# Kernel tuning notes

Hardware: AMD Instinct MI355X
Metric: run time of the kernel (lower is better)

## Reference

```python
import jax, jax.numpy as jnp
import numpy as np

M, N, E, IN, C, HID, TOPK = 4, 50000, 400000, 128, 128, 256, 2
NEG_SLOPE = 0.2


def setup_inputs() -> dict:
    key = jax.random.key(0)
    k = jax.random.split(key, 16)
    s = lambda f: 1.0 / np.sqrt(f)
    return {
        "x_src": jax.random.normal(k[0], (M, N, IN), jnp.float32),
        "x_dst": jax.random.normal(k[1], (N, IN), jnp.float32),
        "src_idx": jax.random.randint(k[2], (M, E), 0, N),
        "dst_idx": jax.random.randint(k[3], (M, E), 0, N),
        "proj_Ws": jax.random.normal(k[4], (M, IN, C), jnp.float32) * s(IN),
        "proj_bs": jnp.zeros((M, C), jnp.float32),
        "projd_W": jax.random.normal(k[5], (IN, C), jnp.float32) * s(IN),
        "projd_b": jnp.zeros((C,), jnp.float32),
        "lin_src": jax.random.normal(k[6], (M, C), jnp.float32) * s(C),
        "lin_dst": jax.random.normal(k[7], (M, C), jnp.float32) * s(C),
        "gm_W1": jax.random.normal(k[8], (C, C), jnp.float32) * s(C),
        "gm_b1": jnp.zeros((C,), jnp.float32),
        "gm_W2": jax.random.normal(k[9], (C, C), jnp.float32) * s(C),
        "gm_b2": jnp.zeros((C,), jnp.float32),
        "gate_W1": jax.random.normal(k[10], (M * C, HID), jnp.float32) * s(M * C),
        "gate_b1": jnp.zeros((HID,), jnp.float32),
        "gate_W2": jax.random.normal(k[11], (HID, M), jnp.float32) * s(HID),
        "gate_b2": jnp.zeros((M,), jnp.float32),
        "exp_W1": jax.random.normal(k[12], (M, C, HID), jnp.float32) * s(C),
        "exp_b1": jnp.zeros((M, HID), jnp.float32),
        "exp_W2": jax.random.normal(k[13], (M, HID, C), jnp.float32) * s(HID),
        "exp_b2": jnp.zeros((M, C), jnp.float32),
    }


def _propagate(xs_t, asrc_t, adst_t, si, di, recept_t):
    # GAT-style attention message passing for one edge type.
    # xs_t: [N,C] projected src feats, asrc_t/adst_t: [N] attn logits,
    # si/di: [E] edge endpoints, recept_t: [N] per-dst-node receptivity gate.
    e = jax.nn.leaky_relu(asrc_t[si] + adst_t[di], NEG_SLOPE)  # [E]
    emax = jax.ops.segment_max(e, di, num_segments=N)
    ez = jnp.exp(e - emax[di])
    den = jax.ops.segment_sum(ez, di, num_segments=N)
    alpha = ez / (den[di] + 1e-16)                             # softmax per dst node
    msg = xs_t[si] * (alpha * recept_t[di])[:, None]           # [E,C]
    return jax.ops.segment_sum(msg, di, num_segments=N)       # [N,C]


def reference(x_src, x_dst, src_idx, dst_idx, proj_Ws, proj_bs, projd_W, projd_b,
              lin_src, lin_dst, gm_W1, gm_b1, gm_W2, gm_b2,
              gate_W1, gate_b1, gate_W2, gate_b2,
              exp_W1, exp_b1, exp_W2, exp_b2):
    # --- SynapticConvLayer (eval path, heads=1) ---
    xs = jnp.einsum('mni,mic->mnc', x_src, proj_Ws) + proj_bs[:, None, :]  # [M,N,C]
    xd = x_dst @ projd_W + projd_b                                          # [N,C]
    a_src = jnp.einsum('mnc,mc->mn', xs, lin_src)
    a_dst = jnp.einsum('nc,mc->mn', xd[None].repeat(M, 0) * 0 + xd[None], lin_dst) if False else jnp.einsum('nc,mc->mn', xd, lin_dst)
    prop = jax.vmap(_propagate)
    out1 = prop(xs, a_src, a_dst, src_idx, dst_idx, jnp.ones((M, N), xs.dtype))
    # receptivity from grad_map surrogate (inference branch)
    feat_diff = out1 - xd[None]                                            # [M,N,C]
    mo = jax.nn.sigmoid(jax.nn.relu(feat_diff @ gm_W1 + gm_b1) @ gm_W2 + gm_b2)
    gd = (mo * feat_diff).mean(axis=-1)                                    # [M,N]
    recept = gd / (jnp.abs(gd) + 1e-8)                                     # L2-norm over the singleton head dim == abs
    out2 = prop(xs, a_src, a_dst, src_idx, dst_idx, recept)
    feats = jax.nn.relu(out2)                                              # [M,N,C] per-edge-type dst features
    # --- SourceExpertMoE ---
    feats_nm = feats.transpose(1, 0, 2)                                    # [N,M,C]
    gate_in = feats_nm.reshape(N, M * C)
    logits = jax.nn.relu(gate_in @ gate_W1 + gate_b1) @ gate_W2 + gate_b2
    gw = jax.nn.softmax(logits, axis=1)
    scores = gw + recept.T                                                 # gate weights + receptivity
    top_w, top_i = jax.lax.top_k(scores, TOPK)
    top_w = top_w / top_w.sum(axis=1, keepdims=True)
    # expert e applied to source-e features for every node (dense, then gather top-k)
    h = jax.nn.relu(jnp.einsum('nmi,mih->nmh', feats_nm, exp_W1) + exp_b1)
    out_all = jnp.einsum('nmh,mho->nmo', h, exp_W2) + exp_b2               # [N,M,C]
    sel = jnp.take_along_axis(out_all, top_i[:, :, None], axis=1)          # [N,K,C]
    final = (sel * top_w[:, :, None]).sum(axis=1)                          # [N,C]
    return final
```

## Files before the change

kernel.cpp:

```cpp
#include <hip/hip_runtime.h>
#include <hip/hip_bf16.h>
#include <math.h>

#define M_  4
#define N_  50000
#define E_  400000
#define IN_ 128
#define C_  128
#define HID_ 256

template<int AMODE, int EPI, int ASCALE>
__global__ void __launch_bounds__(256) gemm7(
    const float* A, const float* A2, const float* __restrict__ B,
    const float* __restrict__ bias, float* Cmat,
    const float* __restrict__ rowscale, const int* __restrict__ idx,
    const int* __restrict__ cnts, const float* __restrict__ AS,
    const float* __restrict__ fdbuf,
    int R, int K, int NC,
    long long aBatch, long long bBatch, int biasBatch, long long cBatch,
    long long strideM)
{
  __shared__ float As[8][128];
  __shared__ float Bs[8][128];
  __shared__ float red[(EPI == 5) ? 128 * 17 : 1];

  const int tid = threadIdx.x;
  const int b = blockIdx.y;
  const int Reff = cnts ? cnts[0] : R;
  const int rb = blockIdx.x * 128;
  if (rb >= Reff) return;
  const int cb = blockIdx.z * 128;

  const float* Ab = (AMODE == 2) ? A : (A + (long long)b * aBatch);
  const float* Bb = B + (long long)b * bBatch + cb;
  const float* biasb = bias + (long long)b * biasBatch + cb;

  const int ar = tid >> 1;
  const int ak = (tid & 1) * 4;
  const int r_a = rb + ar;
  const bool a_ok = (r_a < Reff);
  long long a_row = 0;
  float a_rs = 0.f;
  if (a_ok) {
    if (AMODE == 3) {
      int orow = idx[r_a];
      a_row = (long long)orow * K;
      if (ASCALE == 2) a_rs = AS[orow];
    }
    else if (AMODE == 2) a_row = (long long)r_a * 128;
    else                 a_row = (long long)r_a * K;
  }
  const int bk = tid >> 5;
  const int bc = (tid & 31) * 4;

  const int tx = tid & 15;
  const int ty = tid >> 4;

  float acc[8][8];
  #pragma unroll
  for (int i = 0; i < 8; ++i)
    #pragma unroll
    for (int j = 0; j < 8; ++j) acc[i][j] = 0.f;

  const int nt = K >> 3;
  float4 av = make_float4(0.f, 0.f, 0.f, 0.f), bv;

  if (a_ok) {
    if (AMODE == 2) {
      av = *(const float4*)(Ab + (long long)(ak >> 7) * strideM + a_row + (ak & 127));
      if (ASCALE == 1) {
        float rs = AS[(ak >> 7) * N_ + r_a];
        av.x = fmaxf(av.x * rs, 0.f); av.y = fmaxf(av.y * rs, 0.f);
        av.z = fmaxf(av.z * rs, 0.f); av.w = fmaxf(av.w * rs, 0.f);
      }
    } else {
      av = *(const float4*)(Ab + a_row + ak);
      if (AMODE == 1) {
        float4 y = *(const float4*)(A2 + (long long)r_a * 128 + ak);
        av.x -= y.x; av.y -= y.y; av.z -= y.z; av.w -= y.w;
      }
      if (AMODE == 3 && ASCALE == 2) {
        av.x = fmaxf(av.x * a_rs, 0.f); av.y = fmaxf(av.y * a_rs, 0.f);
        av.z = fmaxf(av.z * a_rs, 0.f); av.w = fmaxf(av.w * a_rs, 0.f);
      }
    }
  }
  bv = *(const float4*)(Bb + (long long)bk * NC + bc);

  for (int t = 0; t < nt; ++t) {
    __syncthreads();
    As[ak + 0][ar] = av.x; As[ak + 1][ar] = av.y;
    As[ak + 2][ar] = av.z; As[ak + 3][ar] = av.w;
    *(float4*)(&Bs[bk][bc]) = bv;
    __syncthreads();

    if (t + 1 < nt) {
      const int k0 = (t + 1) * 8;
      if (a_ok) {
        if (AMODE == 2) {
          int kk0 = k0 + ak;
          av = *(const float4*)(Ab + (long long)(kk0 >> 7) * strideM + a_row + (kk0 & 127));
          if (ASCALE == 1) {
            float rs = AS[(kk0 >> 7) * N_ + r_a];
            av.x = fmaxf(av.x * rs, 0.f); av.y = fmaxf(av.y * rs, 0.f);
            av.z = fmaxf(av.z * rs, 0.f); av.w = fmaxf(av.w * rs, 0.f);
          }
        } else {
          av = *(const float4*)(Ab + a_row + k0 + ak);
          if (AMODE == 1) {
            float4 y = *(const float4*)(A2 + (long long)r_a * 128 + k0 + ak);
            av.x -= y.x; av.y -= y.y; av.z -= y.z; av.w -= y.w;
          }
          if (AMODE == 3 && ASCALE == 2) {
            av.x = fmaxf(av.x * a_rs, 0.f); av.y = fmaxf(av.y * a_rs, 0.f);
            av.z = fmaxf(av.z * a_rs, 0.f); av.w = fmaxf(av.w * a_rs, 0.f);
          }
        }
      }
      bv = *(const float4*)(Bb + (long long)(k0 + bk) * NC + bc);
    }

    #pragma unroll
    for (int kk = 0; kk < 8; ++kk) {
      float4 alo = *(float4*)(&As[kk][ty * 4]);
      float4 ahi = *(float4*)(&As[kk][64 + ty * 4]);
      float4 blo = *(float4*)(&Bs[kk][tx * 4]);
      float4 bhi = *(float4*)(&Bs[kk][64 + tx * 4]);
      float a8[8] = {alo.x, alo.y, alo.z, alo.w, ahi.x, ahi.y, ahi.z, ahi.w};
      float b8[8] = {blo.x, blo.y, blo.z, blo.w, bhi.x, bhi.y, bhi.z, bhi.w};
      #pragma unroll
      for (int i = 0; i < 8; ++i)
        #pragma unroll
        for (int j = 0; j < 8; ++j)
          acc[i][j] += a8[i] * b8[j];
    }
  }

  if (EPI == 5) {
    #pragma unroll
    for (int i = 0; i < 8; ++i) {
      const int r_local = (i < 4 ? ty * 4 + i : 64 + ty * 4 + (i - 4));
      const int r = rb + r_local;
      if (r < Reff) {
        const float* fdrow = fdbuf + (long long)b * cBatch + (long long)r * 128;
        const float* xdrow = A2 + (long long)r * 128;
        float4 flo = *(const float4*)(fdrow + tx * 4);
        float4 fhi = *(const float4*)(fdrow + 64 + tx * 4);
        float4 xlo = *(const float4*)(xdrow + tx * 4);
        float4 xhi = *(const float4*)(xdrow + 64 + tx * 4);
        float fd8[8] = {flo.x - xlo.x, flo.y - xlo.y, flo.z - xlo.z, flo.w - xlo.w,
                        fhi.x - xhi.x, fhi.y - xhi.y, fhi.z - xhi.z, fhi.w - xhi.w};
        float p = 0.f;
        #pragma unroll
        for (int j = 0; j < 8; ++j) {
          const int c = (j < 4 ? tx * 4 + j : 64 + tx * 4 + (j - 4));
          float mo = 1.f / (1.f + expf(-(acc[i][j] + biasb[c])));
          p += mo * fd8[j];
        }
        red[r_local * 17 + tx] = p;
      }
    }
    __syncthreads();
    if (tid < 128) {
      const int r = rb + tid;
      if (r < Reff) {
        float s = 0.f;
        #pragma unroll
        for (int t = 0; t < 16; ++t) s += red[tid * 17 + t];
        float gd = s / 128.f;
        Cmat[(long long)b * N_ + r] = gd / (fabsf(gd) + 1e-8f);
      }
    }
    return;
  }

  #pragma unroll
  for (int i = 0; i < 8; ++i) {
    const int r = rb + (i < 4 ? ty * 4 + i : 64 + ty * 4 + (i - 4));
    if (r >= Reff) continue;
    long long crow;
    float w = 0.f;
    if (EPI == 4) {
      int orow = idx[r];
      w = rowscale[orow];
      crow = (long long)orow * NC + cb;
    } else {
      crow = (long long)b * cBatch + (long long)r * NC + cb;
    }
    #pragma unroll
    for (int j = 0; j < 8; ++j) {
      const int c = (j < 4 ? tx * 4 + j : 64 + tx * 4 + (j - 4));
      float v = acc[i][j] + biasb[c];
      if (EPI == 1) v = fmaxf(v, 0.f);
      if (EPI == 2) v = 1.f / (1.f + expf(-v));
      if (EPI == 4) Cmat[crow + c] += w * v;
      else          Cmat[crow + c] = v;
    }
  }
}

__global__ void attn_logit_kernel(const float* __restrict__ X, const float* __restrict__ lin,
                                  float* __restrict__ out, int Nn, int perM)
{
  int m = blockIdx.y;
  int w = blockIdx.x * (blockDim.x >> 6) + (threadIdx.x >> 6);
  int lane = threadIdx.x & 63;
  if (w >= Nn) return;
  long long row = perM ? ((long long)m * Nn + w) : (long long)w;
  const float* xr = X + row * 128;
  const float* lr = lin + m * 128;
  float acc = xr[lane] * lr[lane] + xr[lane + 64] * lr[lane + 64];
  #pragma unroll
  for (int off = 32; off > 0; off >>= 1) acc += __shfl_down(acc, off);
  if (lane == 0) out[(long long)m * Nn + w] = acc;
}

__global__ void count_kernel(const int* __restrict__ dst, int* __restrict__ cnt, int Nn)
{
  int e = blockIdx.x * blockDim.x + threadIdx.x;
  int m = blockIdx.y;
  if (e >= E_) return;
  atomicAdd(&cnt[(long long)m * Nn + dst[(long long)m * E_ + e]], 1);
}

__global__ void chunkscan_kernel(const int* __restrict__ cnt, int* __restrict__ rowptr,
                                 int* __restrict__ chunktot)
{
  int m = blockIdx.y, ch = blockIdx.x;
  int base = ch * 1024;
  const int* c = cnt + (long long)m * N_;
  int* rp = rowptr + (long long)m * (N_ + 1);
  __shared__ int sums[256];
  int t = threadIdx.x;
  int v[4]; int s = 0;
  #pragma unroll
  for (int k = 0; k < 4; ++k) {
    int i = base + t * 4 + k;
    v[k] = (i < N_) ? c[i] : 0;
    s += v[k];
  }
  sums[t] = s;
  __syncthreads();
  for (int off = 1; off < 256; off <<= 1) {
    int x = (t >= off) ? sums[t - off] : 0;
    __syncthreads();
    sums[t] += x;
    __syncthreads();
  }
  int run = sums[t] - s;
  #pragma unroll
  for (int k = 0; k < 4; ++k) {
    int i = base + t * 4 + k;
    run += v[k];
    if (i < N_) rp[i + 1] = run;
  }
  if (t == 255) chunktot[m * 64 + ch] = sums[255];
}

__global__ void scantot_kernel(int* __restrict__ chunktot, int nch)
{
  int m = threadIdx.x;
  if (m >= M_) return;
  int run = 0;
  for (int ch = 0; ch < nch; ++ch) {
    int v = chunktot[m * 64 + ch];
    chunktot[m * 64 + ch] = run;
    run += v;
  }
}

__global__ void addoff_kernel(int* __restrict__ rowptr, const int* __restrict__ chunktot)
{
  int m = blockIdx.y, ch = blockIdx.x;
  int off = chunktot[m * 64 + ch];
  int t = threadIdx.x;
  int* rp = rowptr + (long long)m * (N_ + 1);
  #pragma unroll
  for (int k = 0; k < 4; ++k) {
    int i = ch * 1024 + t * 4 + k;
    if (i < N_) rp[i + 1] += off;
  }
  if (ch == 0 && t == 0) rp[0] = 0;
}

__global__ void scatter_kernel(const int* __restrict__ dst, const int* __restrict__ rowptr,
                               int* __restrict__ fill, int* __restrict__ col, int Nn)
{
  int e = blockIdx.x * blockDim.x + threadIdx.x;
  int m = blockIdx.y;
  if (e >= E_) return;
  int d = dst[(long long)m * E_ + e];
  int pos = rowptr[(long long)m * (Nn + 1) + d] + atomicAdd(&fill[(long long)m * Nn + d], 1);
  col[(long long)m * E_ + pos] = e;
}

__global__ void sortbucket_kernel(const int* __restrict__ rowptr, int* __restrict__ col, int Nn)
{
  int n = blockIdx.x * blockDim.x + threadIdx.x;
  int m = blockIdx.y;
  if (n >= Nn) return;
  const int* rp = rowptr + (long long)m * (Nn + 1);
  int* c = col + (long long)m * E_;
  int b = rp[n], e = rp[n + 1];
  for (int i = b + 1; i < e; ++i) {
    int v = c[i]; int j = i - 1;
    while (j >= b && c[j] > v) { c[j + 1] = c[j]; --j; }
    c[j + 1] = v;
  }
}

__global__ void edge_e_kernel(const int* __restrict__ src, const int* __restrict__ dst,
                              const float* __restrict__ asrc, const float* __restrict__ adst,
                              float* __restrict__ e_edge)
{
  int e = blockIdx.x * blockDim.x + threadIdx.x;
  int m = blockIdx.y;
  if (e >= E_) return;
  long long off = (long long)m * E_ + e;
  float v = asrc[(long long)m * N_ + src[off]] + adst[(long long)m * N_ + dst[off]];
  e_edge[off] = (v >= 0.f) ? v : 0.2f * v;
}

__global__ void alpha_kernel(const int* __restrict__ rowptr, const int* __restrict__ col,
                             const int* __restrict__ src, const float* __restrict__ e_edge,
                             float* __restrict__ alpha, int* __restrict__ src_csr)
{
  int n = blockIdx.x * blockDim.x + threadIdx.x;
  int m = blockIdx.y;
  if (n >= N_) return;
  const int* rp = rowptr + (long long)m * (N_ + 1);
  const int* cl = col + (long long)m * E_;
  const int* sr = src + (long long)m * E_;
  const float* ee = e_edge + (long long)m * E_;
  float* al = alpha + (long long)m * E_;
  int* sc = src_csr + (long long)m * E_;
  int b = rp[n], en = rp[n + 1];
  if (b == en) return;
  float emax = -INFINITY;
  for (int j = b; j < en; ++j) emax = fmaxf(emax, ee[cl[j]]);
  float den = 0.f;
  for (int j = b; j < en; ++j) {
    int eid = cl[j];
    float ez = expf(ee[eid] - emax);
    den += ez;
    al[j] = ez;
    sc[j] = sr[eid];
  }
  float inv = 1.f / (den + 1e-16f);
  for (int j = b; j < en; ++j) al[j] *= inv;
}

__global__ void prop2_kernel(const float* __restrict__ xs, const int* __restrict__ rowptr,
                             const float* __restrict__ alpha, const int* __restrict__ src_csr,
                             float* __restrict__ out)
{
  int d = blockIdx.x * 2 + (threadIdx.x >> 7);
  int m = blockIdx.y;
  int c = threadIdx.x & 127;
  if (d >= N_) return;
  const int* rp = rowptr + (long long)m * (N_ + 1);
  const float* al = alpha + (long long)m * E_;
  const int* sc = src_csr + (long long)m * E_;
  const float* xsm = xs + (long long)m * N_ * 128;
  int b = rp[d], en = rp[d + 1];
  float acc = 0.f;
  int j = b;
  for (; j + 3 < en; j += 4) {
    float a0 = al[j], a1 = al[j + 1], a2 = al[j + 2], a3 = al[j + 3];
    int s0 = sc[j], s1 = sc[j + 1], s2 = sc[j + 2], s3 = sc[j + 3];
    float x0 = xsm[(long long)s0 * 128 + c];
    float x1 = xsm[(long long)s1 * 128 + c];
    float x2 = xsm[(long long)s2 * 128 + c];
    float x3 = xsm[(long long)s3 * 128 + c];
    acc += a0 * x0; acc += a1 * x1; acc += a2 * x2; acc += a3 * x3;
  }
  for (; j < en; ++j)
    acc += al[j] * xsm[(long long)sc[j] * 128 + c];
  out[((long long)m * N_ + d) * 128 + c] = acc;
}

__global__ void gate_logits_kernel(const float* __restrict__ h, const float* __restrict__ W2,
                                   const float* __restrict__ b2, float* __restrict__ logits, int Nn)
{
  int w = blockIdx.x * (blockDim.x >> 6) + (threadIdx.x >> 6);
  int lane = threadIdx.x & 63;
  if (w >= Nn) return;
  const float* hr = h + (long long)w * 256;
  float a0 = 0.f, a1 = 0.f, a2 = 0.f, a3 = 0.f;
  for (int j = lane; j < 256; j += 64) {
    float hv = hr[j];
    a0 += hv * W2[j * 4 + 0];
    a1 += hv * W2[j * 4 + 1];
    a2 += hv * W2[j * 4 + 2];
    a3 += hv * W2[j * 4 + 3];
  }
  #pragma unroll
  for (int off = 32; off > 0; off >>= 1) {
    a0 += __shfl_down(a0, off);
    a1 += __shfl_down(a1, off);
    a2 += __shfl_down(a2, off);
    a3 += __shfl_down(a3, off);
  }
  if (lane == 0) {
    long long o = (long long)w * 4;
    logits[o + 0] = a0 + b2[0];
    logits[o + 1] = a1 + b2[1];
    logits[o + 2] = a2 + b2[2];
    logits[o + 3] = a3 + b2[3];
  }
}

__global__ void topk_kernel(const float* __restrict__ logits, const float* __restrict__ recept,
                            float* __restrict__ wsel, int Nn)
{
  int n = blockIdx.x * blockDim.x + threadIdx.x;
  if (n >= Nn) return;
  float l[4];
  #pragma unroll
  for (int m = 0; m < 4; ++m) l[m] = logits[(long long)n * 4 + m];
  float mx = fmaxf(fmaxf(l[0], l[1]), fmaxf(l[2], l[3]));
  float e[4], s = 0.f;
  #pragma unroll
  for (int m = 0; m < 4; ++m) { e[m] = expf(l[m] - mx); s += e[m]; }
  float sc[4];
  #pragma unroll
  for (int m = 0; m < 4; ++m) sc[m] = e[m] / s + recept[(long long)m * Nn + n];
  int i0 = 0; float v0 = sc[0];
  #pragma unroll
  for (int m = 1; m < 4; ++m) if (sc[m] > v0) { v0 = sc[m]; i0 = m; }
  int i1 = -1; float v1 = -INFINITY;
  #pragma unroll
  for (int m = 0; m < 4; ++m) { if (m == i0) continue; if (sc[m] > v1) { v1 = sc[m]; i1 = m; } }
  float ts = v0 + v1;
  float w0 = v0 / ts, w1 = v1 / ts;
  #pragma unroll
  for (int m = 0; m < 4; ++m)
    wsel[(long long)m * Nn + n] = (m == i0) ? w0 : ((m == i1) ? w1 : 0.f);
}

__global__ void compact_kernel(const float* __restrict__ wsel, int* __restrict__ idx,
                               int* __restrict__ cnts, int Nn)
{
  int n = blockIdx.x * blockDim.x + threadIdx.x;
  if (n >= Nn) return;
  #pragma unroll
  for (int m = 0; m < 4; ++m) {
    if (wsel[(long long)m * Nn + n] != 0.f) {
      int p = atomicAdd(&cnts[m], 1);
      idx[(long long)m * Nn + p] = n;
    }
  }
}

extern "C" void kernel_launch(void* const* d_in, const int* in_sizes, int n_in,
                              void* d_out, int out_size, void* d_ws, size_t ws_size,
                              hipStream_t stream) {
  const float* x_src   = (const float*)d_in[0];
  const float* x_dst   = (const float*)d_in[1];
  const int*   src_idx = (const int*)d_in[2];
  const int*   dst_idx = (const int*)d_in[3];
  const float* proj_Ws = (const float*)d_in[4];
  const float* proj_bs = (const float*)d_in[5];
  const float* projd_W = (const float*)d_in[6];
  const float* projd_b = (const float*)d_in[7];
  const float* lin_src = (const float*)d_in[8];
  const float* lin_dst = (const float*)d_in[9];
  const float* gm_W1   = (const float*)d_in[10];
  const float* gm_b1   = (const float*)d_in[11];
  const float* gm_W2   = (const float*)d_in[12];
  const float* gm_b2   = (const float*)d_in[13];
  const float* gate_W1 = (const float*)d_in[14];
  const float* gate_b1 = (const float*)d_in[15];
  const float* gate_W2 = (const float*)d_in[16];
  const float* gate_b2 = (const float*)d_in[17];
  const float* exp_W1  = (const float*)d_in[18];
  const float* exp_b1  = (const float*)d_in[19];
  const float* exp_W2  = (const float*)d_in[20];
  const float* exp_b2  = (const float*)d_in[21];
  float* final_out = (float*)d_out;

  float* ws = (float*)d_ws;
  float* bufA   = ws;
  float* bufB   = ws + 25600000LL;
  float* xd     = ws + 51200000LL;
  float* asrc   = ws + 57600000LL;
  float* adst   = ws + 57800000LL;
  float* recept = ws + 58000000LL;
  float* wsel   = ws + 58200000LL;
  float* logits = ws + 58400000LL;
  float* e_edge = ws + 58600000LL;
  float* alpha  = ws + 60200000LL;
  int*   ibase  = (int*)(ws + 61800000LL);
  int*   rowptr = ibase;
  int*   col    = ibase + 200004;
  int*   cnt    = ibase + 1800004;
  int*   expidx = cnt;
  int*   expcnt = ibase + 2000004;
  int*   src_csr= ibase + 2000008;
  int*   chunktot = ibase + 3600008;

  const long long NC = (long long)N_ * C_;
  const int RB = (N_ + 127) / 128;
  const int NCH = (N_ + 1023) / 1024;

  hipMemsetAsync(d_out, 0, (size_t)out_size * sizeof(float), stream);

  hipMemsetAsync(cnt, 0, (size_t)M_ * N_ * sizeof(int), stream);
  count_kernel<<<dim3((E_ + 255) / 256, M_), 256, 0, stream>>>(dst_idx, cnt, N_);
  chunkscan_kernel<<<dim3(NCH, M_), 256, 0, stream>>>(cnt, rowptr, chunktot);
  scantot_kernel<<<1, 64, 0, stream>>>(chunktot, NCH);
  addoff_kernel<<<dim3(NCH, M_), 256, 0, stream>>>(rowptr, chunktot);
  hipMemsetAsync(cnt, 0, (size_t)M_ * N_ * sizeof(int), stream);
  scatter_kernel<<<dim3((E_ + 255) / 256, M_), 256, 0, stream>>>(dst_idx, rowptr, cnt, col, N_);
  sortbucket_kernel<<<dim3((N_ + 255) / 256, M_), 256, 0, stream>>>(rowptr, col, N_);

  gemm7<0, 0, 0><<<dim3(RB, 1, 1), 256, 0, stream>>>(
      x_dst, nullptr, projd_W, projd_b, xd, nullptr, nullptr, nullptr, nullptr, nullptr,
      N_, IN_, C_, 0, 0, 0, 0, 0);
  attn_logit_kernel<<<dim3((N_ + 3) / 4, M_), 256, 0, stream>>>(xd, lin_dst, adst, N_, 0);

  gemm7<0, 0, 0><<<dim3(RB, M_, 1), 256, 0, stream>>>(
      x_src, nullptr, proj_Ws, proj_bs, bufA, nullptr, nullptr, nullptr, nullptr, nullptr,
      N_, IN_, C_, NC, (long long)IN_ * C_, C_, NC, 0);
  attn_logit_kernel<<<dim3((N_ + 3) / 4, M_), 256, 0, stream>>>(bufA, lin_src, asrc, N_, 1);

  edge_e_kernel<<<dim3((E_ + 255) / 256, M_), 256, 0, stream>>>(
      src_idx, dst_idx, asrc, adst, e_edge);
  alpha_kernel<<<dim3((N_ + 255) / 256, M_), 256, 0, stream>>>(
      rowptr, col, src_idx, e_edge, alpha, src_csr);

  prop2_kernel<<<dim3((N_ + 1) / 2, M_), 256, 0, stream>>>(bufA, rowptr, alpha, src_csr, bufB);

  gemm7<1, 1, 0><<<dim3(RB, M_, 1), 256, 0, stream>>>(
      bufB, xd, gm_W1, gm_b1, bufA, nullptr, nullptr, nullptr, nullptr, nullptr,
      N_, C_, C_, NC, 0, 0, NC, 0);
  gemm7<0, 5, 0><<<dim3(RB, M_, 1), 256, 0, stream>>>(
      bufA, xd, gm_W2, gm_b2, recept, nullptr, nullptr, nullptr, nullptr, bufB,
      N_, C_, C_, NC, 0, 0, NC, 0);

  gemm7<2, 1, 1><<<dim3(RB, 1, 2), 256, 0, stream>>>(
      bufB, nullptr, gate_W1, gate_b1, bufA, nullptr, nullptr, nullptr, recept, nullptr,
      N_, M_ * C_, HID_, 0, 0, 0, 0, NC);
  gate_logits_kernel<<<dim3((N_ + 3) / 4), 256, 0, stream>>>(bufA, gate_W2, gate_b2, logits, N_);
  topk_kernel<<<(N_ + 255) / 256, 256, 0, stream>>>(logits, recept, wsel, N_);

  hipMemsetAsync(expcnt, 0, 4 * sizeof(int), stream);
  compact_kernel<<<(N_ + 255) / 256, 256, 0, stream>>>(wsel, expidx, expcnt, N_);

  for (int m = 0; m < M_; ++m) {
    gemm7<3, 1, 2><<<dim3(RB, 1, 2), 256, 0, stream>>>(
        bufB + m * NC, nullptr, exp_W1 + (long long)m * C_ * HID_,
        exp_b1 + (long long)m * HID_, bufA, nullptr,
        expidx + (long long)m * N_, expcnt + m, recept + (long long)m * N_, nullptr,
        N_, C_, HID_, 0, 0, 0, 0, 0);
    gemm7<0, 4, 0><<<dim3(RB, 1, 1), 256, 0, stream>>>(
        bufA, nullptr, exp_W2 + (long long)m * HID_ * C_,
        exp_b2 + (long long)m * C_, final_out, wsel + (long long)m * N_,
        expidx + (long long)m * N_, expcnt + m, nullptr, nullptr,
        N_, HID_, C_, 0, 0, 0, 0, 0);
  }
}
```

Before: 1.381 ms.

## Batch all four expert MLPs into two grouped GEMM launches

Replaces the per-expert loop of eight GEMM launches with two grouped launches that cover all experts through the grid y dimension. Each expert's hidden rows are packed contiguously using a device-side prefix of the expert counts, and the second GEMM accumulates into the output with atomicAdd because experts now run concurrently. This removes launch serialization and small-grid underutilization, at the cost of atomic adds in the epilogue and many early-exit blocks, since each expert gets a full-size grid.

```diff
diff --git a/kernel.cpp b/kernel.cpp
--- a/kernel.cpp
+++ b/kernel.cpp
@@ -10,12 +10,12 @@
 #define HID_ 256
 
 template<int AMODE, int EPI, int ASCALE>
-__global__ void __launch_bounds__(256) gemm7(
+__global__ void __launch_bounds__(256) gemm8(
     const float* A, const float* A2, const float* __restrict__ B,
     const float* __restrict__ bias, float* Cmat,
     const float* __restrict__ rowscale, const int* __restrict__ idx,
     const int* __restrict__ cnts, const float* __restrict__ AS,
-    const float* __restrict__ fdbuf,
+    const float* __restrict__ fdbuf, const int* __restrict__ roff,
     int R, int K, int NC,
     long long aBatch, long long bBatch, int biasBatch, long long cBatch,
     long long strideM)
@@ -26,7 +26,7 @@
 
   const int tid = threadIdx.x;
   const int b = blockIdx.y;
-  const int Reff = cnts ? cnts[0] : R;
+  const int Reff = (AMODE == 4 || AMODE == 5) ? cnts[b] : (cnts ? cnts[0] : R);
   const int rb = blockIdx.x * 128;
   if (rb >= Reff) return;
   const int cb = blockIdx.z * 128;
@@ -46,9 +46,17 @@
       int orow = idx[r_a];
       a_row = (long long)orow * K;
       if (ASCALE == 2) a_rs = AS[orow];
-    }
-    else if (AMODE == 2) a_row = (long long)r_a * 128;
-    else                 a_row = (long long)r_a * K;
+    } else if (AMODE == 4) {
+      int orow = idx[(long long)b * N_ + r_a];
+      a_row = (long long)orow * K;
+      if (ASCALE == 2) a_rs = AS[(long long)b * N_ + orow];
+    } else if (AMODE == 5) {
+      a_row = (long long)(roff[b] + r_a) * K;
+    } else if (AMODE == 2) {
+      a_row = (long long)r_a * 128;
+    } else {
+      a_row = (long long)r_a * K;
+    }
   }
   const int bk = tid >> 5;
   const int bc = (tid & 31) * 4;
@@ -79,7 +87,7 @@
         float4 y = *(const float4*)(A2 + (long long)r_a * 128 + ak);
         av.x -= y.x; av.y -= y.y; av.z -= y.z; av.w -= y.w;
       }
-      if (AMODE == 3 && ASCALE == 2) {
+      if ((AMODE == 3 || AMODE == 4) && ASCALE == 2) {
         av.x = fmaxf(av.x * a_rs, 0.f); av.y = fmaxf(av.y * a_rs, 0.f);
         av.z = fmaxf(av.z * a_rs, 0.f); av.w = fmaxf(av.w * a_rs, 0.f);
       }
@@ -111,7 +119,7 @@
             float4 y = *(const float4*)(A2 + (long long)r_a * 128 + k0 + ak);
             av.x -= y.x; av.y -= y.y; av.z -= y.z; av.w -= y.w;
           }
-          if (AMODE == 3 && ASCALE == 2) {
+          if ((AMODE == 3 || AMODE == 4) && ASCALE == 2) {
             av.x = fmaxf(av.x * a_rs, 0.f); av.y = fmaxf(av.y * a_rs, 0.f);
             av.z = fmaxf(av.z * a_rs, 0.f); av.w = fmaxf(av.w * a_rs, 0.f);
           }
@@ -184,6 +192,12 @@
       int orow = idx[r];
       w = rowscale[orow];
       crow = (long long)orow * NC + cb;
+    } else if (EPI == 8) {
+      int orow = idx[(long long)b * N_ + r];
+      w = rowscale[(long long)b * N_ + orow];
+      crow = (long long)orow * 128 + cb;
+    } else if (EPI == 7) {
+      crow = (long long)(roff[b] + r) * NC + cb;
     } else {
       crow = (long long)b * cBatch + (long long)r * NC + cb;
     }
@@ -191,10 +205,11 @@
     for (int j = 0; j < 8; ++j) {
       const int c = (j < 4 ? tx * 4 + j : 64 + tx * 4 + (j - 4));
       float v = acc[i][j] + biasb[c];
-      if (EPI == 1) v = fmaxf(v, 0.f);
+      if (EPI == 1 || EPI == 7) v = fmaxf(v, 0.f);
       if (EPI == 2) v = 1.f / (1.f + expf(-v));
       if (EPI == 4) Cmat[crow + c] += w * v;
-      else          Cmat[crow + c] = v;
+      else if (EPI == 8) atomicAdd(&Cmat[crow + c], w * v);
+      else Cmat[crow + c] = v;
     }
   }
 }
@@ -449,6 +464,15 @@
       int p = atomicAdd(&cnts[m], 1);
       idx[(long long)m * Nn + p] = n;
     }
+  }
+}
+
+__global__ void prefix4_kernel(const int* __restrict__ cnts, int* __restrict__ off)
+{
+  if (threadIdx.x == 0) {
+    int r = 0;
+    #pragma unroll
+    for (int m = 0; m < 4; ++m) { off[m] = r; r += cnts[m]; }
   }
 }
 
@@ -498,6 +522,7 @@
   int*   expcnt = ibase + 2000004;
   int*   src_csr= ibase + 2000008;
   int*   chunktot = ibase + 3600008;
+  int*   expoff = ibase + 3600264;
 
   const long long NC = (long long)N_ * C_;
   const int RB = (N_ + 127) / 128;
@@ -514,14 +539,14 @@
   scatter_kernel<<<dim3((E_ + 255) / 256, M_), 256, 0, stream>>>(dst_idx, rowptr, cnt, col, N_);
   sortbucket_kernel<<<dim3((N_ + 255) / 256, M_), 256, 0, stream>>>(rowptr, col, N_);
 
-  gemm7<0, 0, 0><<<dim3(RB, 1, 1), 256, 0, stream>>>(
+  gemm8<0, 0, 0><<<dim3(RB, 1, 1), 256, 0, stream>>>(
       x_dst, nullptr, projd_W, projd_b, xd, nullptr, nullptr, nullptr, nullptr, nullptr,
-      N_, IN_, C_, 0, 0, 0, 0, 0);
+      nullptr, N_, IN_, C_, 0, 0, 0, 0, 0);
   attn_logit_kernel<<<dim3((N_ + 3) / 4, M_), 256, 0, stream>>>(xd, lin_dst, adst, N_, 0);
 
-  gemm7<0, 0, 0><<<dim3(RB, M_, 1), 256, 0, stream>>>(
+  gemm8<0, 0, 0><<<dim3(RB, M_, 1), 256, 0, stream>>>(
       x_src, nullptr, proj_Ws, proj_bs, bufA, nullptr, nullptr, nullptr, nullptr, nullptr,
-      N_, IN_, C_, NC, (long long)IN_ * C_, C_, NC, 0);
+      nullptr, N_, IN_, C_, NC, (long long)IN_ * C_, C_, NC, 0);
   attn_logit_kernel<<<dim3((N_ + 3) / 4, M_), 256, 0, stream>>>(bufA, lin_src, asrc, N_, 1);
 
   edge_e_kernel<<<dim3((E_ + 255) / 256, M_), 256, 0, stream>>>(
@@ -531,32 +556,29 @@
 
   prop2_kernel<<<dim3((N_ + 1) / 2, M_), 256, 0, stream>>>(bufA, rowptr, alpha, src_csr, bufB);
 
-  gemm7<1, 1, 0><<<dim3(RB, M_, 1), 256, 0, stream>>>(
+  gemm8<1, 1, 0><<<dim3(RB, M_, 1), 256, 0, stream>>>(
       bufB, xd, gm_W1, gm_b1, bufA, nullptr, nullptr, nullptr, nullptr, nullptr,
-      N_, C_, C_, NC, 0, 0, NC, 0);
-  gemm7<0, 5, 0><<<dim3(RB, M_, 1), 256, 0, stream>>>(
+      nullptr, N_, C_, C_, NC, 0, 0, NC, 0);
+  gemm8<0, 5, 0><<<dim3(RB, M_, 1), 256, 0, stream>>>(
       bufA, xd, gm_W2, gm_b2, recept, nullptr, nullptr, nullptr, nullptr, bufB,
-      N_, C_, C_, NC, 0, 0, NC, 0);
-
-  gemm7<2, 1, 1><<<dim3(RB, 1, 2), 256, 0, stream>>>(
+      nullptr, N_, C_, C_, NC, 0, 0, NC, 0);
+
+  gemm8<2, 1, 1><<<dim3(RB, 1, 2), 256, 0, stream>>>(
       bufB, nullptr, gate_W1, gate_b1, bufA, nullptr, nullptr, nullptr, recept, nullptr,
-      N_, M_ * C_, HID_, 0, 0, 0, 0, NC);
+      nullptr, N_, M_ * C_, HID_, 0, 0, 0, 0, NC);
   gate_logits_kernel<<<dim3((N_ + 3) / 4), 256, 0, stream>>>(bufA, gate_W2, gate_b2, logits, N_);
   topk_kernel<<<(N_ + 255) / 256, 256, 0, stream>>>(logits, recept, wsel, N_);
 
   hipMemsetAsync(expcnt, 0, 4 * sizeof(int), stream);
   compact_kernel<<<(N_ + 255) / 256, 256, 0, stream>>>(wsel, expidx, expcnt, N_);
-
-  for (int m = 0; m < M_; ++m) {
-    gemm7<3, 1, 2><<<dim3(RB, 1, 2), 256, 0, stream>>>(
-        bufB + m * NC, nullptr, exp_W1 + (long long)m * C_ * HID_,
-        exp_b1 + (long long)m * HID_, bufA, nullptr,
-        expidx + (long long)m * N_, expcnt + m, recept + (long long)m * N_, nullptr,
-        N_, C_, HID_, 0, 0, 0, 0, 0);
-    gemm7<0, 4, 0><<<dim3(RB, 1, 1), 256, 0, stream>>>(
-        bufA, nullptr, exp_W2 + (long long)m * HID_ * C_,
-        exp_b2 + (long long)m * C_, final_out, wsel + (long long)m * N_,
-        expidx + (long long)m * N_, expcnt + m, nullptr, nullptr,
-        N_, HID_, C_, 0, 0, 0, 0, 0);
-  }
-}
+  prefix4_kernel<<<1, 64, 0, stream>>>(expcnt, expoff);
+
+  gemm8<4, 7, 2><<<dim3(RB, M_, 2), 256, 0, stream>>>(
+      bufB, nullptr, exp_W1, exp_b1, bufA, nullptr,
+      expidx, expcnt, recept, nullptr, expoff,
+      N_, C_, HID_, NC, (long long)C_ * HID_, HID_, 0, 0);
+  gemm8<5, 8, 0><<<dim3(RB, M_, 1), 256, 0, stream>>>(
+      bufA, nullptr, exp_W2, exp_b2, final_out, wsel,
+      expidx, expcnt, nullptr, nullptr, expoff,
+      N_, HID_, C_, 0, (long long)HID_ * C_, C_, 0, 0);
+}
```

Result: no change. 1.379 ms (-0.1%).
